# Optimization experiments

Hardware: AMD Instinct MI355X
Metric: run time of the kernel (lower is better)

The kernel has to match this reference:

```python
import jax, jax.numpy as jnp
import numpy as np

D_MODEL = 256
D_EDGE = 64
EPS = 1e-05
INPUT_FEATS = 2 * D_MODEL + D_EDGE + 1  # 577


def _linear_params(key, fan_in, fan_out):
    k1, k2 = jax.random.split(key)
    lim = 1.0 / np.sqrt(fan_in)
    W = jax.random.uniform(k1, (fan_in, fan_out), minval=-lim, maxval=lim, dtype=jnp.float32)
    b = jax.random.uniform(k2, (fan_out,), minval=-lim, maxval=lim, dtype=jnp.float32)
    return W, b


def setup_inputs() -> dict:
    key = jax.random.key(0)
    ks = jax.random.split(key, 16)
    B, N = 8, 128
    inp = {
        "coords": jax.random.normal(ks[0], (B, N, 3), dtype=jnp.float32),
        "inv_feats": jax.random.normal(ks[1], (B, N, D_MODEL), dtype=jnp.float32),
        "adj_matrix": jnp.ones((B, N, N), dtype=jnp.float32),
        "atom_mask": jnp.ones((B, N), dtype=jnp.float32),
        "edge_feats": jax.random.normal(ks[2], (B, N, N, D_EDGE), dtype=jnp.float32),
    }
    inp["W_e1"], inp["b_e1"] = _linear_params(ks[3], INPUT_FEATS, D_MODEL)
    inp["W_e2"], inp["b_e2"] = _linear_params(ks[4], D_MODEL, D_MODEL)
    inp["W_att"], inp["b_att"] = _linear_params(ks[5], D_MODEL, 1)
    inp["W_h1"], inp["b_h1"] = _linear_params(ks[6], 2 * D_MODEL, D_MODEL)
    inp["W_h2"], inp["b_h2"] = _linear_params(ks[7], D_MODEL, D_MODEL)
    inp["W_x1"], inp["b_x1"] = _linear_params(ks[8], INPUT_FEATS, D_MODEL)
    inp["W_x2"], inp["b_x2"] = _linear_params(ks[9], D_MODEL, D_MODEL)
    inp["W_x3"], inp["b_x3"] = _linear_params(ks[10], D_MODEL, 1)
    return inp


def _pair_linear(W, b, node_feats, ef):
    # Linear over concat([node_i, node_j, ef]) without materializing the concat.
    # W: [2*d_model + d_edge + 1, out]
    d = D_MODEL
    hi = node_feats @ W[:d]          # [B,N,out]
    hj = node_feats @ W[d:2 * d]     # [B,N,out]
    he = ef @ W[2 * d:]              # [B,N,N,out]
    return hi[:, :, None, :] + hj[:, None, :, :] + he + b


def _egnn_forward(coords, inv_feats, adj_matrix, atom_mask, edge_feats,
                  W_e1, b_e1, W_e2, b_e2, W_att, b_att,
                  W_h1, b_h1, W_h2, b_h2, W_x1, b_x1, W_x2, b_x2, W_x3, b_x3):
    mask = atom_mask[..., None]                       # [B,N,1]
    diff = coords[:, :, None, :] - coords[:, None, :, :]   # [B,N,N,3]
    sq = jnp.sum(diff * diff, axis=-1, keepdims=True)      # [B,N,N,1]
    ef = jnp.concatenate([edge_feats, sq], axis=-1)        # [B,N,N,d_edge+1]
    adj = adj_matrix[..., None]                             # [B,N,N,1]

    # phi_e: Linear-SiLU-Linear-SiLU on pair features
    msg = jax.nn.silu(_pair_linear(W_e1, b_e1, inv_feats, ef))
    msg = jax.nn.silu(msg @ W_e2 + b_e2)                    # [B,N,N,d]

    att = jax.nn.sigmoid(msg @ W_att + b_att)               # [B,N,N,1]
    node_msg = jnp.sum(msg * att * adj, axis=2)             # [B,N,d]

    h = jnp.concatenate([inv_feats, node_msg], axis=-1)
    h = jax.nn.silu(h @ W_h1 + b_h1) @ W_h2 + b_h2          # [B,N,d]

    # phi_x: Linear-SiLU-Linear-SiLU-Linear -> scalar per edge
    ex = jax.nn.silu(_pair_linear(W_x1, b_x1, inv_feats, ef))
    ex = jax.nn.silu(ex @ W_x2 + b_x2)
    edge_attn = ex @ W_x3 + b_x3                             # [B,N,N,1]

    normalisers = jnp.sqrt(sq[..., 0] + EPS) + 1.0           # [B,N,N]
    weighted = diff * edge_attn / normalisers[..., None] * adj
    coord_updates = jnp.sum(weighted, axis=2)                # [B,N,3]
    num_nodes = jnp.sum(mask, axis=1) + 1.0                  # [B,1]
    coord_updates = coord_updates / num_nodes[:, :, None]

    out_coords = (coords + coord_updates) * mask
    out_feats = h * mask
    return out_coords, out_feats


def reference(coords, inv_feats, adj_matrix, atom_mask, edge_feats,
              W_e1, b_e1, W_e2, b_e2, W_att, b_att,
              W_h1, b_h1, W_h2, b_h2, W_x1, b_x1, W_x2, b_x2, W_x3, b_x3):
    return _egnn_forward(coords, inv_feats, adj_matrix, atom_mask, edge_feats,
                         W_e1, b_e1, W_e2, b_e2, W_att, b_att,
                         W_h1, b_h1, W_h2, b_h2, W_x1, b_x1, W_x2, b_x2, W_x3, b_x3)
```

## Files before the change

kernel.cpp:

```cpp
#include <hip/hip_runtime.h>

typedef __attribute__((ext_vector_type(8))) __bf16 bf16x8;
typedef __attribute__((ext_vector_type(4))) __bf16 bf16x4;
typedef __attribute__((ext_vector_type(4))) float f32x4;

#define SCHED0 __builtin_amdgcn_sched_barrier(0)

__device__ __forceinline__ float fast_sig(float x) {
  return __builtin_amdgcn_rcpf(1.0f + __expf(-x));
}
__device__ __forceinline__ float siluf(float x) { return x * fast_sig(x); }
__device__ __forceinline__ __bf16 tobf(float x) { return (__bf16)x; }

__device__ __forceinline__ void stage16(const void* g, void* l) {
  __builtin_amdgcn_global_load_lds(
      (const __attribute__((address_space(1))) void*)g,
      (__attribute__((address_space(3))) void*)l, 16, 0, 0);
}

__device__ __forceinline__ void stage_pw(
    const __bf16* __restrict__ src, int ld, int off,
    __bf16* dst, int lane, int cg)
{
  #pragma unroll
  for (int q = 0; q < 2; q++) {
    const __bf16* g = src + (size_t)(cg + q * 16 + (lane & 15)) * ld + off + (lane >> 4) * 8;
    stage16(g, dst + q * 512);
  }
}

__device__ __forceinline__ void stage_pw_k(
    const __bf16* __restrict__ wt, const __bf16* __restrict__ w2,
    int k, __bf16* dst, int lane, int cg)
{
  if (k < 2) stage_pw(wt, 576, 512 + k * 32, dst, lane, cg);
  else       stage_pw(w2, 256, (k - 2) * 32, dst, lane, cg);
}

__global__ __launch_bounds__(256) void k_prep(
    const float* __restrict__ We1, const float* __restrict__ Wx1,
    const float* __restrict__ We2, const float* __restrict__ Wx2,
    const float* __restrict__ Wh1, const float* __restrict__ Wh2,
    const float* __restrict__ invf,
    __bf16* __restrict__ wt_e, __bf16* __restrict__ wt_x,
    __bf16* __restrict__ w2e, __bf16* __restrict__ w2x,
    __bf16* __restrict__ wh1t, __bf16* __restrict__ wh2t,
    __bf16* __restrict__ invb,
    float* __restrict__ nmsg, float* __restrict__ cupd)
{
  int idx = blockIdx.x * 256 + threadIdx.x;
  if (idx < 147456) {
    int kk = idx / 576, f = idx - kk * 576;
    wt_e[idx] = tobf(We1[f * 256 + kk]);
    wt_x[idx] = tobf(Wx1[f * 256 + kk]);
  }
  if (idx < 65536) {
    int c = idx >> 8, k = idx & 255;
    w2e[idx] = tobf(We2[k * 256 + c]);
    w2x[idx] = tobf(Wx2[k * 256 + c]);
    wh2t[idx] = tobf(Wh2[k * 256 + c]);
    f32x4 z = {0.f, 0.f, 0.f, 0.f};
    *(f32x4*)(nmsg + idx * 4) = z;
  }
  if (idx < 131072) {
    int c = idx >> 9, k = idx & 511;
    wh1t[idx] = tobf(Wh1[k * 256 + c]);
  }
  if (idx < 3072) cupd[idx] = 0.f;
  invb[idx] = tobf(invf[idx]);
}

template<int NKS>
__device__ __forceinline__ void node_gemm64(
    const __bf16* __restrict__ B, int ldb, int boff,
    const __bf16* __restrict__ A, int lda, int aoff,
    int row0, int tid, f32x4 acc[4][4])
{
  const int lane = tid & 63, wc = tid >> 6, lr = lane & 15, lg = lane >> 4;
  #pragma unroll
  for (int ks = 0; ks < NKS; ks++) {
    bf16x8 bB[4], aA[4];
    #pragma unroll
    for (int m = 0; m < 4; m++)
      bB[m] = *(const bf16x8*)(B + (size_t)(row0 + m * 16 + lr) * ldb + boff + ks * 32 + lg * 8);
    #pragma unroll
    for (int n = 0; n < 4; n++)
      aA[n] = *(const bf16x8*)(A + (size_t)(wc * 64 + n * 16 + lr) * lda + aoff + ks * 32 + lg * 8);
    #pragma unroll
    for (int m = 0; m < 4; m++)
      #pragma unroll
      for (int n = 0; n < 4; n++)
        acc[m][n] = __builtin_amdgcn_mfma_f32_16x16x32_bf16(aA[n], bB[m], acc[m][n], 0, 0, 0);
  }
}

__global__ __launch_bounds__(256) void k_nproj(
    const __bf16* __restrict__ invb,
    const __bf16* __restrict__ wt_e, const __bf16* __restrict__ wt_x,
    const float* __restrict__ be1, const float* __restrict__ bx1,
    float* __restrict__ hie, float* __restrict__ hix,
    __bf16* __restrict__ hje, __bf16* __restrict__ hjx)
{
  const int tid = threadIdx.x;
  const int row0 = blockIdx.x * 64;
  const int mat = blockIdx.y;
  const __bf16* A = (mat < 2) ? wt_e : wt_x;
  const int aoff = (mat & 1) ? 256 : 0;

  f32x4 acc[4][4];
  #pragma unroll
  for (int m = 0; m < 4; m++)
    #pragma unroll
    for (int n = 0; n < 4; n++) { f32x4 z = {0.f,0.f,0.f,0.f}; acc[m][n] = z; }
  node_gemm64<8>(invb, 256, 0, A, 576, aoff, row0, tid, acc);

  const int lane = tid & 63, wc = tid >> 6, lr = lane & 15, lg = lane >> 4;
  if ((mat & 1) == 0) {
    const float* bias = (mat == 0) ? be1 : bx1;
    float* out = (mat == 0) ? hie : hix;
    #pragma unroll
    for (int m = 0; m < 4; m++) {
      int node = row0 + m * 16 + lr;
      #pragma unroll
      for (int n = 0; n < 4; n++) {
        int c0 = wc * 64 + n * 16 + lg * 4;
        f32x4 v = acc[m][n] + *(const f32x4*)(bias + c0);
        *(f32x4*)(out + (size_t)node * 256 + c0) = v;
      }
    }
  } else {
    __bf16* out = (mat == 1) ? hje : hjx;
    #pragma unroll
    for (int m = 0; m < 4; m++) {
      int node = row0 + m * 16 + lr;
      #pragma unroll
      for (int n = 0; n < 4; n++) {
        int c0 = wc * 64 + n * 16 + lg * 4;
        bf16x4 pk;
        #pragma unroll
        for (int r = 0; r < 4; r++) pk[r] = tobf(acc[m][n][r]);
        *(bf16x4*)(out + (size_t)node * 256 + c0) = pk;
      }
    }
  }
}

__global__ __launch_bounds__(256) void k_h1(
    const __bf16* __restrict__ invb, const float* __restrict__ nmsg,
    const __bf16* __restrict__ wh1t,
    const float* __restrict__ bh1, __bf16* __restrict__ h1b)
{
  const int tid = threadIdx.x;
  const int row0 = blockIdx.x * 64;
  const int c0 = blockIdx.y * 64;
  const int lane = tid & 63, w = tid >> 6, lr = lane & 15, lg = lane >> 4;
  const int node = row0 + w * 16 + lr;

  f32x4 acc[4];
  #pragma unroll
  for (int n = 0; n < 4; n++) { f32x4 z = {0.f,0.f,0.f,0.f}; acc[n] = z; }

  #pragma unroll
  for (int ks = 0; ks < 16; ks++) {
    bf16x8 bB;
    if (ks < 8) {
      bB = *(const bf16x8*)(invb + (size_t)node * 256 + ks * 32 + lg * 8);
    } else {
      const float* pp = nmsg + (size_t)node * 256 + (ks - 8) * 32 + lg * 8;
      f32x4 lo = *(const f32x4*)pp;
      f32x4 hi = *(const f32x4*)(pp + 4);
      bf16x8 t;
      t[0]=tobf(lo[0]); t[1]=tobf(lo[1]); t[2]=tobf(lo[2]); t[3]=tobf(lo[3]);
      t[4]=tobf(hi[0]); t[5]=tobf(hi[1]); t[6]=tobf(hi[2]); t[7]=tobf(hi[3]);
      bB = t;
    }
    #pragma unroll
    for (int n = 0; n < 4; n++) {
      bf16x8 aA = *(const bf16x8*)(wh1t + (size_t)(c0 + n * 16 + lr) * 512 + ks * 32 + lg * 8);
      acc[n] = __builtin_amdgcn_mfma_f32_16x16x32_bf16(aA, bB, acc[n], 0, 0, 0);
    }
  }

  #pragma unroll
  for (int n = 0; n < 4; n++) {
    int cc = c0 + n * 16 + lg * 4;
    f32x4 b4 = *(const f32x4*)(bh1 + cc);
    bf16x4 pk;
    #pragma unroll
    for (int r = 0; r < 4; r++) pk[r] = tobf(siluf(acc[n][r] + b4[r]));
    *(bf16x4*)(h1b + (size_t)node * 256 + cc) = pk;
  }
}

__global__ __launch_bounds__(256) void k_h2(
    const __bf16* __restrict__ h1b, const __bf16* __restrict__ wh2t,
    const float* __restrict__ bh2, const float* __restrict__ amask,
    const float* __restrict__ coords, const float* __restrict__ cupd,
    float* __restrict__ out_feats, float* __restrict__ out_coords)
{
  __shared__ float sM[2];
  const int tid = threadIdx.x;
  const int row0 = blockIdx.x * 64;
  const int c0 = blockIdx.y * 64;
  const int b = row0 >> 7;
  const int lane = tid & 63, w = tid >> 6, lr = lane & 15, lg = lane >> 4;
  const int node = row0 + w * 16 + lr;

  f32x4 acc[4];
  #pragma unroll
  for (int n = 0; n < 4; n++) { f32x4 z = {0.f,0.f,0.f,0.f}; acc[n] = z; }

  #pragma unroll
  for (int ks = 0; ks < 8; ks++) {
    bf16x8 bB = *(const bf16x8*)(h1b + (size_t)node * 256 + ks * 32 + lg * 8);
    #pragma unroll
    for (int n = 0; n < 4; n++) {
      bf16x8 aA = *(const bf16x8*)(wh2t + (size_t)(c0 + n * 16 + lr) * 256 + ks * 32 + lg * 8);
      acc[n] = __builtin_amdgcn_mfma_f32_16x16x32_bf16(aA, bB, acc[n], 0, 0, 0);
    }
  }

  float msk = amask[node];
  #pragma unroll
  for (int n = 0; n < 4; n++) {
    int cc = c0 + n * 16 + lg * 4;
    f32x4 b4 = *(const f32x4*)(bh2 + cc);
    f32x4 v = (acc[n] + b4) * msk;
    *(f32x4*)(out_feats + (size_t)node * 256 + cc) = v;
  }

  if (blockIdx.y == 0) {
    if (tid < 128) {
      float v = amask[b * 128 + tid];
      #pragma unroll
      for (int off = 1; off < 64; off <<= 1) v += __shfl_xor(v, off);
      if ((tid & 63) == 0) sM[tid >> 6] = v;
    }
    __syncthreads();
    const float sNum = sM[0] + sM[1];
    if (tid < 192) {
      int nl = tid / 3, d = tid - nl * 3;
      int nd = row0 + nl;
      float upd = cupd[nd * 3 + d] / (sNum + 1.0f);
      out_coords[nd * 3 + d] = (coords[nd * 3 + d] + upd) * amask[nd];
    }
  }
}

__global__ __launch_bounds__(512, 4) void k_edge(
    const float* __restrict__ coords, const float* __restrict__ adjm,
    const float* __restrict__ ef,
    const float* __restrict__ We1, const float* __restrict__ Wx1,
    const float* __restrict__ batt,
    const float* __restrict__ be2, const float* __restrict__ bx2,
    const float* __restrict__ bx3,
    const float* __restrict__ Watt, const float* __restrict__ Wx3,
    const float* __restrict__ hie, const float* __restrict__ hix,
    const __bf16* __restrict__ hje, const __bf16* __restrict__ hjx,
    const __bf16* __restrict__ wt_e, const __bf16* __restrict__ wt_x,
    const __bf16* __restrict__ w2e, const __bf16* __restrict__ w2x,
    float* __restrict__ nmsg, float* __restrict__ cupd)
{
  __shared__ __align__(16) char sSb[64 * 512];
  __shared__ __align__(16) __bf16 sW[2][8][1024];
  __shared__ __align__(16) __bf16 sE[64 * 72];
  __shared__ float slaste[256], slastx[256];
  __shared__ float sqv[64], sAdj[64], sRedE[64], sRedX[64], sNM[256], sCup[4];

  const int tid = threadIdx.x;
  const int raw = blockIdx.x;
  const int lb = (raw & 7) * 256 + (raw >> 3);
  const int bi = lb >> 1;
  const int half = lb & 1;
  const int b = bi >> 7;
  const int j0g = half * 64;
  const int jg0 = b * 128 + j0g;

  const int lane = tid & 63;
  const int wv = tid >> 6;
  const int lr = lane & 15, lg = lane >> 4;
  const int cg = wv * 32;

  const float cix = coords[bi * 3 + 0];
  const float ciy = coords[bi * 3 + 1];
  const float ciz = coords[bi * 3 + 2];
  const float b0e = batt[0];
  const float b0x = bx3[0];

  stage_pw(wt_e, 576, 512, &sW[0][wv][0], lane, cg);
  stage_pw(wt_e, 576, 544, &sW[1][wv][0], lane, cg);

  if (tid < 64) { sRedE[tid] = 0.f; sRedX[tid] = 0.f; }
  else if (tid < 320) sNM[tid - 64] = 0.f;
  else if (tid < 324) sCup[tid - 320] = 0.f;
  if (tid < 256) {
    slaste[tid] = We1[576 * 256 + tid];
    slastx[tid] = Wx1[576 * 256 + tid];
  }
  if (tid >= 448) {
    int j = tid - 448;
    int jg = jg0 + j;
    float dx = cix - coords[jg * 3 + 0];
    float dy = ciy - coords[jg * 3 + 1];
    float dz = ciz - coords[jg * 3 + 2];
    sqv[j] = dx * dx + dy * dy + dz * dz;
  }
  if (tid >= 384 && tid < 448)
    sAdj[tid - 384] = adjm[(size_t)bi * 128 + j0g + (tid - 384)];

  {
    const float* efb = ef + ((size_t)bi * 128 + j0g) * 64;
    int row = tid >> 3;
    int col = (tid & 7) * 8;
    const float* er = efb + row * 64 + col;
    f32x4 x = *(const f32x4*)er;
    f32x4 y = *(const f32x4*)(er + 4);
    bf16x8 t;
    t[0] = tobf(x[0]); t[1] = tobf(x[1]); t[2] = tobf(x[2]); t[3] = tobf(x[3]);
    t[4] = tobf(y[0]); t[5] = tobf(y[1]); t[6] = tobf(y[2]); t[7] = tobf(y[3]);
    *(bf16x8*)(sE + row * 72 + col) = t;
  }

  SCHED0;
  asm volatile("s_waitcnt lgkmcnt(0)" ::: "memory");
  __builtin_amdgcn_s_barrier();
  SCHED0;

  #pragma unroll
  for (int p = 0; p < 2; p++) {
    const __bf16* wt = p ? wt_x : wt_e;
    const __bf16* w2 = p ? w2x : w2e;
    const float* hi_g = (p ? hix : hie) + (size_t)bi * 256;
    const __bf16* hj_g = (p ? hjx : hje) + (size_t)jg0 * 256;
    const float* slast = p ? slastx : slaste;
    const float* bias2 = p ? bx2 : be2;
    const float* vvec = p ? Wx3 : Watt;
    float* sRed = p ? sRedX : sRedE;
    const float batt0 = p ? b0x : b0e;

    f32x4 acc[4][2];
    #pragma unroll
    for (int m = 0; m < 4; m++)
      #pragma unroll
      for (int n = 0; n < 2; n++) { f32x4 z = {0.f,0.f,0.f,0.f}; acc[m][n] = z; }

    #pragma unroll
    for (int k = 0; k < 10; k++) {
      SCHED0;
      if (p == 1 && k == 9) asm volatile("s_waitcnt vmcnt(0)" ::: "memory");
      else                  asm volatile("s_waitcnt vmcnt(2)" ::: "memory");
      SCHED0;

      const __bf16* swp = &sW[k & 1][wv][0];
      bf16x8 aW[2];
      #pragma unroll
      for (int n = 0; n < 2; n++)
        aW[n] = *(const bf16x8*)(swp + n * 512 + lg * 128 + lr * 8);

      bf16x8 bX[4];
      if (k < 2) {
        #pragma unroll
        for (int m = 0; m < 4; m++)
          bX[m] = *(const bf16x8*)(sE + (m * 16 + lr) * 72 + k * 32 + lg * 8);
      } else {
        const int ks = k - 2;
        #pragma unroll
        for (int m = 0; m < 4; m++) {
          const int jl = m * 16 + lr;
          int off = (jl * 512 + (ks * 32 + lg * 8) * 2) ^ ((jl & 7) << 4);
          bX[m] = *(const bf16x8*)(sSb + off);
        }
      }

      __builtin_amdgcn_s_setprio(1);
      #pragma unroll
      for (int m = 0; m < 4; m++)
        #pragma unroll
        for (int n = 0; n < 2; n++)
          acc[m][n] = __builtin_amdgcn_mfma_f32_16x16x32_bf16(aW[n], bX[m], acc[m][n], 0, 0, 0);
      __builtin_amdgcn_s_setprio(0);

      if (k == 1) {
        f32x4 hi4[2];
        bf16x4 hj4[4][2];
        #pragma unroll
        for (int n = 0; n < 2; n++)
          hi4[n] = *(const f32x4*)(hi_g + cg + n * 16 + lg * 4);
        #pragma unroll
        for (int m = 0; m < 4; m++) {
          const int jl = m * 16 + lr;
          #pragma unroll
          for (int n = 0; n < 2; n++)
            hj4[m][n] = *(const bf16x4*)(hj_g + (size_t)jl * 256 + cg + n * 16 + lg * 4);
        }
        #pragma unroll
        for (int m = 0; m < 4; m++) {
          const int jl = m * 16 + lr;
          const float sq = sqv[jl];
          #pragma unroll
          for (int n = 0; n < 2; n++) {
            const int kk0 = cg + n * 16 + lg * 4;
            f32x4 sl4 = *(const f32x4*)(slast + kk0);
            bf16x4 pk;
            #pragma unroll
            for (int r = 0; r < 4; r++) {
              float v = acc[m][n][r] + hi4[n][r] + (float)hj4[m][n][r] + sq * sl4[r];
              pk[r] = tobf(siluf(v));
            }
            int off = (jl * 512 + kk0 * 2) ^ ((jl & 7) << 4);
            *(bf16x4*)(sSb + off) = pk;
            f32x4 z = {0.f, 0.f, 0.f, 0.f};
            acc[m][n] = z;
          }
        }
        SCHED0;
        asm volatile("s_waitcnt lgkmcnt(0)" ::: "memory");
        __builtin_amdgcn_s_barrier();
        SCHED0;
      }

      SCHED0;
      asm volatile("s_waitcnt lgkmcnt(0)" ::: "memory");
      SCHED0;
      __bf16* dst = &sW[k & 1][wv][0];
      if (k < 8)       stage_pw_k(wt, w2, k + 2, dst, lane, cg);
      else if (p == 0) stage_pw_k(wt_x, w2x, k - 8, dst, lane, cg);
    }

    float pr[4] = {0.f, 0.f, 0.f, 0.f};
    #pragma unroll
    for (int n = 0; n < 2; n++) {
      f32x4 bb = *(const f32x4*)(bias2 + cg + n * 16 + lg * 4);
      f32x4 vv = *(const f32x4*)(vvec  + cg + n * 16 + lg * 4);
      #pragma unroll
      for (int m = 0; m < 4; m++)
        #pragma unroll
        for (int r = 0; r < 4; r++) {
          float s = siluf(acc[m][n][r] + bb[r]);
          acc[m][n][r] = s;
          pr[m] += s * vv[r];
        }
    }
    #pragma unroll
    for (int m = 0; m < 4; m++) {
      pr[m] += __shfl_xor(pr[m], 16);
      pr[m] += __shfl_xor(pr[m], 32);
    }
    if (lane < 16) {
      #pragma unroll
      for (int m = 0; m < 4; m++)
        atomicAdd(&sRed[m * 16 + lr], pr[m]);
    }
    SCHED0;
    asm volatile("s_waitcnt lgkmcnt(0)" ::: "memory");
    __builtin_amdgcn_s_barrier();
    SCHED0;

    if (p == 0) {
      float aw[4];
      #pragma unroll
      for (int m = 0; m < 4; m++)
        aw[m] = fast_sig(sRed[m * 16 + lr] + batt0) * sAdj[m * 16 + lr];
      f32x4 q[2];
      #pragma unroll
      for (int n = 0; n < 2; n++) { f32x4 z = {0.f,0.f,0.f,0.f}; q[n] = z; }
      #pragma unroll
      for (int m = 0; m < 4; m++)
        #pragma unroll
        for (int n = 0; n < 2; n++)
          q[n] += acc[m][n] * aw[m];
      #pragma unroll
      for (int off = 1; off < 16; off <<= 1)
        #pragma unroll
        for (int n = 0; n < 2; n++)
          #pragma unroll
          for (int r = 0; r < 4; r++)
            q[n][r] += __shfl_xor(q[n][r], off);
      if (lr == 0) {
        #pragma unroll
        for (int n = 0; n < 2; n++)
          #pragma unroll
          for (int r = 0; r < 4; r++)
            atomicAdd(&sNM[cg + n * 16 + lg * 4 + r], q[n][r]);
      }
    } else {
      if (tid < 64) {
        int jl = tid;
        int jgl = jg0 + jl;
        float ea = sRed[jl] + batt0;
        float wgt = ea * __builtin_amdgcn_rcpf(sqrtf(sqv[jl] + 1e-5f) + 1.0f) * sAdj[jl];
        float wx = wgt * (cix - coords[jgl * 3 + 0]);
        float wy = wgt * (ciy - coords[jgl * 3 + 1]);
        float wz = wgt * (ciz - coords[jgl * 3 + 2]);
        #pragma unroll
        for (int off = 1; off < 64; off <<= 1) {
          wx += __shfl_xor(wx, off);
          wy += __shfl_xor(wy, off);
          wz += __shfl_xor(wz, off);
        }
        if (tid == 0) { sCup[0] = wx; sCup[1] = wy; sCup[2] = wz; }
      }
    }
  }

  __syncthreads();
  if (tid < 256) atomicAdd(&nmsg[(size_t)bi * 256 + tid], sNM[tid]);
  if (tid < 3) atomicAdd(&cupd[bi * 3 + tid], sCup[tid]);
}

extern "C" void kernel_launch(void* const* d_in, const int* in_sizes, int n_in,
                              void* d_out, int out_size, void* d_ws, size_t ws_size,
                              hipStream_t stream)
{
  const float* coords = (const float*)d_in[0];
  const float* invf  = (const float*)d_in[1];
  const float* adjm  = (const float*)d_in[2];
  const float* amask = (const float*)d_in[3];
  const float* ef    = (const float*)d_in[4];
  const float* We1   = (const float*)d_in[5];
  const float* be1   = (const float*)d_in[6];
  const float* We2   = (const float*)d_in[7];
  const float* be2   = (const float*)d_in[8];
  const float* Watt  = (const float*)d_in[9];
  const float* batt  = (const float*)d_in[10];
  const float* Wh1   = (const float*)d_in[11];
  const float* bh1   = (const float*)d_in[12];
  const float* Wh2   = (const float*)d_in[13];
  const float* bh2   = (const float*)d_in[14];
  const float* Wx1   = (const float*)d_in[15];
  const float* bx1   = (const float*)d_in[16];
  const float* Wx2   = (const float*)d_in[17];
  const float* bx2   = (const float*)d_in[18];
  const float* Wx3   = (const float*)d_in[19];
  const float* bx3   = (const float*)d_in[20];

  char* ws = (char*)d_ws;
  const size_t MB = 1u << 20;
  float*  hie  = (float*)(ws + 0 * MB);
  float*  hix  = (float*)(ws + 1 * MB);
  __bf16* hje  = (__bf16*)(ws + 2 * MB);
  __bf16* hjx  = (__bf16*)(ws + 2 * MB + 524288);
  __bf16* invb = (__bf16*)(ws + 3 * MB);
  __bf16* h1b  = (__bf16*)(ws + 3 * MB + 524288);
  size_t woff = 4 * MB;
  __bf16* wt_e = (__bf16*)(ws + woff);
  __bf16* wt_x = (__bf16*)(ws + woff + 294912);
  __bf16* w2e  = (__bf16*)(ws + woff + 2 * 294912);
  __bf16* w2x  = (__bf16*)(ws + woff + 2 * 294912 + 131072);
  __bf16* wh1t = (__bf16*)(ws + woff + 2 * 294912 + 2 * 131072);
  __bf16* wh2t = (__bf16*)(ws + woff + 2 * 294912 + 2 * 131072 + 262144);
  float*  nmsg = (float*)(ws + 5 * MB + 524288);
  float*  cupd = (float*)(ws + 6 * MB + 524288);

  float* out_coords = (float*)d_out;
  float* out_feats  = out_coords + 8 * 128 * 3;

  hipLaunchKernelGGL(k_prep, dim3(1024), dim3(256), 0, stream,
                     We1, Wx1, We2, Wx2, Wh1, Wh2, invf,
                     wt_e, wt_x, w2e, w2x, wh1t, wh2t, invb, nmsg, cupd);
  hipLaunchKernelGGL(k_nproj, dim3(16, 4), dim3(256), 0, stream,
                     invb, wt_e, wt_x, be1, bx1, hie, hix, hje, hjx);
  hipLaunchKernelGGL(k_edge, dim3(2048), dim3(512), 0, stream,
                     coords, adjm, ef, We1, Wx1, batt, be2, bx2, bx3, Watt, Wx3,
                     hie, hix, hje, hjx, wt_e, wt_x, w2e, w2x, nmsg, cupd);
  hipLaunchKernelGGL(k_h1, dim3(16, 4), dim3(256), 0, stream,
                     invb, nmsg, wh1t, bh1, h1b);
  hipLaunchKernelGGL(k_h2, dim3(16, 4), dim3(256), 0, stream,
                     h1b, wh2t, bh2, amask, coords, cupd, out_feats, out_coords);
}
```

Before: 185.9 us.

## Make edge kernel persistent with register-resident weights, splitting phi_e/phi_x across blocks

The edge kernel now launches 512 blocks, each handling one of the two MLP branches (phi_e or phi_x) for eight consecutive half-rows. The per-wave weight fragments for the edge-feature and second-layer GEMMs are loaded into registers once and reused across all eight tiles, replacing the double-buffered LDS weight streaming. Node-message and coordinate accumulations go straight to global atomics per tile instead of through a block-level LDS reduction. This removes repeated weight staging, but it raises register pressure (occupancy hint drops to 2), loses the overlap between weight loads and MFMA, and adds more global atomics and per-tile barriers.

```diff
diff --git a/kernel.cpp b/kernel.cpp
--- a/kernel.cpp
+++ b/kernel.cpp
@@ -11,31 +11,6 @@
 }
 __device__ __forceinline__ float siluf(float x) { return x * fast_sig(x); }
 __device__ __forceinline__ __bf16 tobf(float x) { return (__bf16)x; }
-
-__device__ __forceinline__ void stage16(const void* g, void* l) {
-  __builtin_amdgcn_global_load_lds(
-      (const __attribute__((address_space(1))) void*)g,
-      (__attribute__((address_space(3))) void*)l, 16, 0, 0);
-}
-
-__device__ __forceinline__ void stage_pw(
-    const __bf16* __restrict__ src, int ld, int off,
-    __bf16* dst, int lane, int cg)
-{
-  #pragma unroll
-  for (int q = 0; q < 2; q++) {
-    const __bf16* g = src + (size_t)(cg + q * 16 + (lane & 15)) * ld + off + (lane >> 4) * 8;
-    stage16(g, dst + q * 512);
-  }
-}
-
-__device__ __forceinline__ void stage_pw_k(
-    const __bf16* __restrict__ wt, const __bf16* __restrict__ w2,
-    int k, __bf16* dst, int lane, int cg)
-{
-  if (k < 2) stage_pw(wt, 576, 512 + k * 32, dst, lane, cg);
-  else       stage_pw(w2, 256, (k - 2) * 32, dst, lane, cg);
-}
 
 __global__ __launch_bounds__(256) void k_prep(
     const float* __restrict__ We1, const float* __restrict__ Wx1,
@@ -247,7 +222,7 @@
   }
 }
 
-__global__ __launch_bounds__(512, 4) void k_edge(
+__global__ __launch_bounds__(512, 2) void k_edge(
     const float* __restrict__ coords, const float* __restrict__ adjm,
     const float* __restrict__ ef,
     const float* __restrict__ We1, const float* __restrict__ Wx1,
@@ -262,205 +237,182 @@
     float* __restrict__ nmsg, float* __restrict__ cupd)
 {
   __shared__ __align__(16) char sSb[64 * 512];
-  __shared__ __align__(16) __bf16 sW[2][8][1024];
   __shared__ __align__(16) __bf16 sE[64 * 72];
-  __shared__ float slaste[256], slastx[256];
-  __shared__ float sqv[64], sAdj[64], sRedE[64], sRedX[64], sNM[256], sCup[4];
+  __shared__ float sqv[64], sAdj[2][64], sRed[2][64];
 
   const int tid = threadIdx.x;
-  const int raw = blockIdx.x;
-  const int lb = (raw & 7) * 256 + (raw >> 3);
-  const int bi = lb >> 1;
-  const int half = lb & 1;
-  const int b = bi >> 7;
-  const int j0g = half * 64;
-  const int jg0 = b * 128 + j0g;
-
+  const int p = blockIdx.x & 1;
+  const int widx = blockIdx.x >> 1;
   const int lane = tid & 63;
   const int wv = tid >> 6;
   const int lr = lane & 15, lg = lane >> 4;
   const int cg = wv * 32;
 
-  const float cix = coords[bi * 3 + 0];
-  const float ciy = coords[bi * 3 + 1];
-  const float ciz = coords[bi * 3 + 2];
-  const float b0e = batt[0];
-  const float b0x = bx3[0];
-
-  stage_pw(wt_e, 576, 512, &sW[0][wv][0], lane, cg);
-  stage_pw(wt_e, 576, 544, &sW[1][wv][0], lane, cg);
-
-  if (tid < 64) { sRedE[tid] = 0.f; sRedX[tid] = 0.f; }
-  else if (tid < 320) sNM[tid - 64] = 0.f;
-  else if (tid < 324) sCup[tid - 320] = 0.f;
-  if (tid < 256) {
-    slaste[tid] = We1[576 * 256 + tid];
-    slastx[tid] = Wx1[576 * 256 + tid];
-  }
-  if (tid >= 448) {
-    int j = tid - 448;
-    int jg = jg0 + j;
-    float dx = cix - coords[jg * 3 + 0];
-    float dy = ciy - coords[jg * 3 + 1];
-    float dz = ciz - coords[jg * 3 + 2];
-    sqv[j] = dx * dx + dy * dy + dz * dz;
-  }
-  if (tid >= 384 && tid < 448)
-    sAdj[tid - 384] = adjm[(size_t)bi * 128 + j0g + (tid - 384)];
-
-  {
-    const float* efb = ef + ((size_t)bi * 128 + j0g) * 64;
-    int row = tid >> 3;
-    int col = (tid & 7) * 8;
-    const float* er = efb + row * 64 + col;
-    f32x4 x = *(const f32x4*)er;
-    f32x4 y = *(const f32x4*)(er + 4);
-    bf16x8 t;
-    t[0] = tobf(x[0]); t[1] = tobf(x[1]); t[2] = tobf(x[2]); t[3] = tobf(x[3]);
-    t[4] = tobf(y[0]); t[5] = tobf(y[1]); t[6] = tobf(y[2]); t[7] = tobf(y[3]);
-    *(bf16x8*)(sE + row * 72 + col) = t;
-  }
-
-  SCHED0;
-  asm volatile("s_waitcnt lgkmcnt(0)" ::: "memory");
-  __builtin_amdgcn_s_barrier();
-  SCHED0;
-
-  #pragma unroll
-  for (int p = 0; p < 2; p++) {
-    const __bf16* wt = p ? wt_x : wt_e;
-    const __bf16* w2 = p ? w2x : w2e;
-    const float* hi_g = (p ? hix : hie) + (size_t)bi * 256;
-    const __bf16* hj_g = (p ? hjx : hje) + (size_t)jg0 * 256;
-    const float* slast = p ? slastx : slaste;
-    const float* bias2 = p ? bx2 : be2;
-    const float* vvec = p ? Wx3 : Watt;
-    float* sRed = p ? sRedX : sRedE;
-    const float batt0 = p ? b0x : b0e;
-
-    f32x4 acc[4][2];
-    #pragma unroll
-    for (int m = 0; m < 4; m++)
-      #pragma unroll
-      for (int n = 0; n < 2; n++) { f32x4 z = {0.f,0.f,0.f,0.f}; acc[m][n] = z; }
-
-    #pragma unroll
-    for (int k = 0; k < 10; k++) {
-      SCHED0;
-      if (p == 1 && k == 9) asm volatile("s_waitcnt vmcnt(0)" ::: "memory");
-      else                  asm volatile("s_waitcnt vmcnt(2)" ::: "memory");
-      SCHED0;
-
-      const __bf16* swp = &sW[k & 1][wv][0];
-      bf16x8 aW[2];
-      #pragma unroll
-      for (int n = 0; n < 2; n++)
-        aW[n] = *(const bf16x8*)(swp + n * 512 + lg * 128 + lr * 8);
-
-      bf16x8 bX[4];
-      if (k < 2) {
-        #pragma unroll
-        for (int m = 0; m < 4; m++)
-          bX[m] = *(const bf16x8*)(sE + (m * 16 + lr) * 72 + k * 32 + lg * 8);
-      } else {
-        const int ks = k - 2;
-        #pragma unroll
-        for (int m = 0; m < 4; m++) {
-          const int jl = m * 16 + lr;
-          int off = (jl * 512 + (ks * 32 + lg * 8) * 2) ^ ((jl & 7) << 4);
-          bX[m] = *(const bf16x8*)(sSb + off);
-        }
-      }
-
-      __builtin_amdgcn_s_setprio(1);
-      #pragma unroll
-      for (int m = 0; m < 4; m++)
-        #pragma unroll
-        for (int n = 0; n < 2; n++)
-          acc[m][n] = __builtin_amdgcn_mfma_f32_16x16x32_bf16(aW[n], bX[m], acc[m][n], 0, 0, 0);
-      __builtin_amdgcn_s_setprio(0);
-
-      if (k == 1) {
-        f32x4 hi4[2];
-        bf16x4 hj4[4][2];
-        #pragma unroll
-        for (int n = 0; n < 2; n++)
-          hi4[n] = *(const f32x4*)(hi_g + cg + n * 16 + lg * 4);
-        #pragma unroll
-        for (int m = 0; m < 4; m++) {
-          const int jl = m * 16 + lr;
-          #pragma unroll
-          for (int n = 0; n < 2; n++)
-            hj4[m][n] = *(const bf16x4*)(hj_g + (size_t)jl * 256 + cg + n * 16 + lg * 4);
-        }
-        #pragma unroll
-        for (int m = 0; m < 4; m++) {
-          const int jl = m * 16 + lr;
-          const float sq = sqv[jl];
-          #pragma unroll
-          for (int n = 0; n < 2; n++) {
-            const int kk0 = cg + n * 16 + lg * 4;
-            f32x4 sl4 = *(const f32x4*)(slast + kk0);
-            bf16x4 pk;
-            #pragma unroll
-            for (int r = 0; r < 4; r++) {
-              float v = acc[m][n][r] + hi4[n][r] + (float)hj4[m][n][r] + sq * sl4[r];
-              pk[r] = tobf(siluf(v));
-            }
-            int off = (jl * 512 + kk0 * 2) ^ ((jl & 7) << 4);
-            *(bf16x4*)(sSb + off) = pk;
-            f32x4 z = {0.f, 0.f, 0.f, 0.f};
-            acc[m][n] = z;
-          }
-        }
-        SCHED0;
-        asm volatile("s_waitcnt lgkmcnt(0)" ::: "memory");
-        __builtin_amdgcn_s_barrier();
-        SCHED0;
-      }
-
-      SCHED0;
-      asm volatile("s_waitcnt lgkmcnt(0)" ::: "memory");
-      SCHED0;
-      __bf16* dst = &sW[k & 1][wv][0];
-      if (k < 8)       stage_pw_k(wt, w2, k + 2, dst, lane, cg);
-      else if (p == 0) stage_pw_k(wt_x, w2x, k - 8, dst, lane, cg);
-    }
-
-    float pr[4] = {0.f, 0.f, 0.f, 0.f};
-    #pragma unroll
-    for (int n = 0; n < 2; n++) {
-      f32x4 bb = *(const f32x4*)(bias2 + cg + n * 16 + lg * 4);
-      f32x4 vv = *(const f32x4*)(vvec  + cg + n * 16 + lg * 4);
-      #pragma unroll
-      for (int m = 0; m < 4; m++)
-        #pragma unroll
-        for (int r = 0; r < 4; r++) {
-          float s = siluf(acc[m][n][r] + bb[r]);
-          acc[m][n][r] = s;
-          pr[m] += s * vv[r];
-        }
-    }
-    #pragma unroll
-    for (int m = 0; m < 4; m++) {
-      pr[m] += __shfl_xor(pr[m], 16);
-      pr[m] += __shfl_xor(pr[m], 32);
-    }
-    if (lane < 16) {
-      #pragma unroll
-      for (int m = 0; m < 4; m++)
-        atomicAdd(&sRed[m * 16 + lr], pr[m]);
+  const __bf16* wt = p ? wt_x : wt_e;
+  const __bf16* w2 = p ? w2x : w2e;
+  const float* hi_mat = p ? hix : hie;
+  const __bf16* hj_mat = p ? hjx : hje;
+  const float* slast_g = (p ? Wx1 : We1) + 576 * 256;
+  const float b0 = p ? bx3[0] : batt[0];
+
+  f32x4 bb[2], vv[2], sl[2];
+  #pragma unroll
+  for (int n = 0; n < 2; n++) {
+    bb[n] = *(const f32x4*)((p ? bx2 : be2) + cg + n * 16 + lg * 4);
+    vv[n] = *(const f32x4*)((p ? Wx3 : Watt) + cg + n * 16 + lg * 4);
+    sl[n] = *(const f32x4*)(slast_g + cg + n * 16 + lg * 4);
+  }
+
+  bf16x8 aW1[2][2], aW2[8][2];
+  #pragma unroll
+  for (int ks = 0; ks < 2; ks++)
+    #pragma unroll
+    for (int n = 0; n < 2; n++)
+      aW1[ks][n] = *(const bf16x8*)(wt + (size_t)(cg + n * 16 + lr) * 576 + 512 + ks * 32 + lg * 8);
+  #pragma unroll
+  for (int ks = 0; ks < 8; ks++)
+    #pragma unroll
+    for (int n = 0; n < 2; n++)
+      aW2[ks][n] = *(const bf16x8*)(w2 + (size_t)(cg + n * 16 + lr) * 256 + ks * 32 + lg * 8);
+
+  for (int t = 0; t < 8; ++t) {
+    const int h = widx * 8 + t;
+    const int bi = h >> 1;
+    const int b = bi >> 7;
+    const int jg0 = b * 128 + (h & 1) * 64;
+
+    if (tid < 64) {
+      sRed[t & 1][tid] = 0.f;
+      int jg = jg0 + tid;
+      float dx = coords[bi * 3 + 0] - coords[jg * 3 + 0];
+      float dy = coords[bi * 3 + 1] - coords[jg * 3 + 1];
+      float dz = coords[bi * 3 + 2] - coords[jg * 3 + 2];
+      sqv[tid] = dx * dx + dy * dy + dz * dz;
+    } else if (tid < 128) {
+      sAdj[t & 1][tid - 64] = adjm[(size_t)bi * 128 + (h & 1) * 64 + (tid - 64)];
+    }
+    {
+      const float* efb = ef + ((size_t)bi * 128 + (h & 1) * 64) * 64;
+      int row = tid >> 3, col = (tid & 7) * 8;
+      const float* er = efb + row * 64 + col;
+      f32x4 x = *(const f32x4*)er;
+      f32x4 y = *(const f32x4*)(er + 4);
+      bf16x8 e8;
+      e8[0] = tobf(x[0]); e8[1] = tobf(x[1]); e8[2] = tobf(x[2]); e8[3] = tobf(x[3]);
+      e8[4] = tobf(y[0]); e8[5] = tobf(y[1]); e8[6] = tobf(y[2]); e8[7] = tobf(y[3]);
+      *(bf16x8*)(sE + row * 72 + col) = e8;
     }
     SCHED0;
     asm volatile("s_waitcnt lgkmcnt(0)" ::: "memory");
     __builtin_amdgcn_s_barrier();
     SCHED0;
 
+    f32x4 hi4[2];
+    bf16x4 hj4[4][2];
+    #pragma unroll
+    for (int n = 0; n < 2; n++)
+      hi4[n] = *(const f32x4*)(hi_mat + (size_t)bi * 256 + cg + n * 16 + lg * 4);
+    #pragma unroll
+    for (int m = 0; m < 4; m++)
+      #pragma unroll
+      for (int n = 0; n < 2; n++)
+        hj4[m][n] = *(const bf16x4*)(hj_mat + (size_t)(jg0 + m * 16 + lr) * 256 + cg + n * 16 + lg * 4);
+
+    f32x4 acc[4][2];
+    #pragma unroll
+    for (int m = 0; m < 4; m++)
+      #pragma unroll
+      for (int n = 0; n < 2; n++) { f32x4 z = {0.f,0.f,0.f,0.f}; acc[m][n] = z; }
+
+    #pragma unroll
+    for (int ks = 0; ks < 2; ks++) {
+      bf16x8 bE[4];
+      #pragma unroll
+      for (int m = 0; m < 4; m++)
+        bE[m] = *(const bf16x8*)(sE + (m * 16 + lr) * 72 + ks * 32 + lg * 8);
+      __builtin_amdgcn_s_setprio(1);
+      #pragma unroll
+      for (int m = 0; m < 4; m++)
+        #pragma unroll
+        for (int n = 0; n < 2; n++)
+          acc[m][n] = __builtin_amdgcn_mfma_f32_16x16x32_bf16(aW1[ks][n], bE[m], acc[m][n], 0, 0, 0);
+      __builtin_amdgcn_s_setprio(0);
+    }
+
+    #pragma unroll
+    for (int m = 0; m < 4; m++) {
+      const int jl = m * 16 + lr;
+      const float sq = sqv[jl];
+      #pragma unroll
+      for (int n = 0; n < 2; n++) {
+        const int kk0 = cg + n * 16 + lg * 4;
+        bf16x4 pk;
+        #pragma unroll
+        for (int r = 0; r < 4; r++) {
+          float v = acc[m][n][r] + hi4[n][r] + (float)hj4[m][n][r] + sq * sl[n][r];
+          pk[r] = tobf(siluf(v));
+        }
+        int off = (jl * 512 + kk0 * 2) ^ ((jl & 7) << 4);
+        *(bf16x4*)(sSb + off) = pk;
+        f32x4 z = {0.f, 0.f, 0.f, 0.f};
+        acc[m][n] = z;
+      }
+    }
+    SCHED0;
+    asm volatile("s_waitcnt lgkmcnt(0)" ::: "memory");
+    __builtin_amdgcn_s_barrier();
+    SCHED0;
+
+    #pragma unroll
+    for (int ks = 0; ks < 8; ks++) {
+      bf16x8 bS[4];
+      #pragma unroll
+      for (int m = 0; m < 4; m++) {
+        const int jl = m * 16 + lr;
+        int off = (jl * 512 + (ks * 32 + lg * 8) * 2) ^ ((jl & 7) << 4);
+        bS[m] = *(const bf16x8*)(sSb + off);
+      }
+      __builtin_amdgcn_s_setprio(1);
+      #pragma unroll
+      for (int m = 0; m < 4; m++)
+        #pragma unroll
+        for (int n = 0; n < 2; n++)
+          acc[m][n] = __builtin_amdgcn_mfma_f32_16x16x32_bf16(aW2[ks][n], bS[m], acc[m][n], 0, 0, 0);
+      __builtin_amdgcn_s_setprio(0);
+    }
+
+    float pr[4] = {0.f, 0.f, 0.f, 0.f};
+    #pragma unroll
+    for (int n = 0; n < 2; n++) {
+      #pragma unroll
+      for (int m = 0; m < 4; m++)
+        #pragma unroll
+        for (int r = 0; r < 4; r++) {
+          float s = siluf(acc[m][n][r] + bb[n][r]);
+          acc[m][n][r] = s;
+          pr[m] += s * vv[n][r];
+        }
+    }
+    #pragma unroll
+    for (int m = 0; m < 4; m++) {
+      pr[m] += __shfl_xor(pr[m], 16);
+      pr[m] += __shfl_xor(pr[m], 32);
+    }
+    if (lane < 16) {
+      #pragma unroll
+      for (int m = 0; m < 4; m++)
+        atomicAdd(&sRed[t & 1][m * 16 + lr], pr[m]);
+    }
+    SCHED0;
+    asm volatile("s_waitcnt lgkmcnt(0)" ::: "memory");
+    __builtin_amdgcn_s_barrier();
+    SCHED0;
+
     if (p == 0) {
       float aw[4];
       #pragma unroll
       for (int m = 0; m < 4; m++)
-        aw[m] = fast_sig(sRed[m * 16 + lr] + batt0) * sAdj[m * 16 + lr];
+        aw[m] = fast_sig(sRed[t & 1][m * 16 + lr] + b0) * sAdj[t & 1][m * 16 + lr];
       f32x4 q[2];
       #pragma unroll
       for (int n = 0; n < 2; n++) { f32x4 z = {0.f,0.f,0.f,0.f}; q[n] = z; }
@@ -481,31 +433,31 @@
         for (int n = 0; n < 2; n++)
           #pragma unroll
           for (int r = 0; r < 4; r++)
-            atomicAdd(&sNM[cg + n * 16 + lg * 4 + r], q[n][r]);
+            atomicAdd(&nmsg[(size_t)bi * 256 + cg + n * 16 + lg * 4 + r], q[n][r]);
       }
     } else {
       if (tid < 64) {
         int jl = tid;
         int jgl = jg0 + jl;
-        float ea = sRed[jl] + batt0;
-        float wgt = ea * __builtin_amdgcn_rcpf(sqrtf(sqv[jl] + 1e-5f) + 1.0f) * sAdj[jl];
-        float wx = wgt * (cix - coords[jgl * 3 + 0]);
-        float wy = wgt * (ciy - coords[jgl * 3 + 1]);
-        float wz = wgt * (ciz - coords[jgl * 3 + 2]);
+        float ea = sRed[t & 1][jl] + b0;
+        float wgt = ea * __builtin_amdgcn_rcpf(sqrtf(sqv[jl] + 1e-5f) + 1.0f) * sAdj[t & 1][jl];
+        float wx = wgt * (coords[bi * 3 + 0] - coords[jgl * 3 + 0]);
+        float wy = wgt * (coords[bi * 3 + 1] - coords[jgl * 3 + 1]);
+        float wz = wgt * (coords[bi * 3 + 2] - coords[jgl * 3 + 2]);
         #pragma unroll
         for (int off = 1; off < 64; off <<= 1) {
           wx += __shfl_xor(wx, off);
           wy += __shfl_xor(wy, off);
           wz += __shfl_xor(wz, off);
         }
-        if (tid == 0) { sCup[0] = wx; sCup[1] = wy; sCup[2] = wz; }
+        if (tid == 0) {
+          atomicAdd(&cupd[bi * 3 + 0], wx);
+          atomicAdd(&cupd[bi * 3 + 1], wy);
+          atomicAdd(&cupd[bi * 3 + 2], wz);
+        }
       }
     }
   }
-
-  __syncthreads();
-  if (tid < 256) atomicAdd(&nmsg[(size_t)bi * 256 + tid], sNM[tid]);
-  if (tid < 3) atomicAdd(&cupd[bi * 3 + tid], sCup[tid]);
 }
 
 extern "C" void kernel_launch(void* const* d_in, const int* in_sizes, int n_in,
@@ -560,7 +512,7 @@
                      wt_e, wt_x, w2e, w2x, wh1t, wh2t, invb, nmsg, cupd);
   hipLaunchKernelGGL(k_nproj, dim3(16, 4), dim3(256), 0, stream,
                      invb, wt_e, wt_x, be1, bx1, hie, hix, hje, hjx);
-  hipLaunchKernelGGL(k_edge, dim3(2048), dim3(512), 0, stream,
+  hipLaunchKernelGGL(k_edge, dim3(512), dim3(512), 0, stream,
                      coords, adjm, ef, We1, Wx1, batt, be2, bx2, bx3, Watt, Wx3,
                      hie, hix, hje, hjx, wt_e, wt_x, w2e, w2x, nmsg, cupd);
   hipLaunchKernelGGL(k_h1, dim3(16, 4), dim3(256), 0, stream,
```

Measured after the change: 151.5 us. 18.5% less time.
